# Optimization experiments

Hardware: AMD Instinct MI355X
Metric: run time of the kernel (lower is better)

## Reference

```python
import jax, jax.numpy as jnp
import numpy as np

N_NODES = 50000


def gcn_conv(x, src, dst, W, b):
    """PyG GCNConv: symmetric-normalized aggregation with self-loops.
    out[i] = sum_{j->i} deg^{-1/2}[j] deg^{-1/2}[i] (x_j @ W) + b
    src/dst already include self-loop edges.
    """
    n = x.shape[0]
    ew = jnp.ones(src.shape[0], dtype=x.dtype)
    deg = jax.ops.segment_sum(ew, dst, num_segments=n)  # [N]
    dinv = jnp.where(deg > 0, jax.lax.rsqrt(deg), 0.0).astype(x.dtype)
    norm = dinv[src] * dinv[dst]  # [E+N]
    xw = x @ W  # [N, z] dense transform first (as PyG does)
    msg = xw[src] * norm[:, None]  # gather + scale, [E+N, z]
    out = jax.ops.segment_sum(msg, dst, num_segments=n)  # scatter-add
    return out + b


def prelu(x, a):
    return jnp.where(x > 0, x, a * x)


def setup_inputs() -> dict:
    key = jax.random.key(0)
    k1, k2, k3, k4 = jax.random.split(key, 4)
    in_dim = z_dim = 96
    n_edges = 800000
    x = jax.random.normal(k1, (N_NODES, in_dim), dtype=jnp.float32)
    edge_index = jax.random.randint(k2, (2, n_edges), 0, N_NODES, dtype=jnp.int32)
    # Glorot-style init for GCN weights
    s1 = 1.0 / np.sqrt(in_dim)
    W1 = jax.random.uniform(k3, (in_dim, z_dim), jnp.float32, -s1, s1)
    W2 = jax.random.uniform(k4, (z_dim, z_dim), jnp.float32, -s1, s1)
    b1 = jnp.zeros((z_dim,), jnp.float32)
    b2 = jnp.zeros((z_dim,), jnp.float32)
    prelu_a = jnp.full((z_dim,), 0.25, jnp.float32)  # shared PReLU, per-channel
    return {"x": x, "edge_index": edge_index, "W1": W1, "b1": b1,
            "W2": W2, "b2": b2, "prelu_a": prelu_a}


def reference(x, edge_index, W1, b1, W2, b2, prelu_a):
    n = x.shape[0]
    loop = jnp.arange(n, dtype=edge_index.dtype)
    src = jnp.concatenate([edge_index[0], loop])
    dst = jnp.concatenate([edge_index[1], loop])
    h = prelu(gcn_conv(x, src, dst, W1, b1), prelu_a)
    h = prelu(gcn_conv(h, src, dst, W2, b2), prelu_a)
    return h
```

## Files before the change

### kernel.cpp

```cpp
#include <hip/hip_runtime.h>
#include <hip/hip_fp16.h>

#define D 96
#define D4 24
#define MAXBINS 256

static inline size_t alignup(size_t x) { return (x + 255) & ~size_t(255); }

__device__ inline float4 f4fma(float s, float4 a, float4 acc) {
    acc.x = fmaf(s, a.x, acc.x);
    acc.y = fmaf(s, a.y, acc.y);
    acc.z = fmaf(s, a.z, acc.z);
    acc.w = fmaf(s, a.w, acc.w);
    return acc;
}

__device__ inline void u4fma(uint4 rv, float w, float4& a0, float4& a1) {
    __half2 h0 = *reinterpret_cast<__half2*>(&rv.x);
    __half2 h1 = *reinterpret_cast<__half2*>(&rv.y);
    __half2 h2 = *reinterpret_cast<__half2*>(&rv.z);
    __half2 h3 = *reinterpret_cast<__half2*>(&rv.w);
    float2 f0 = __half22float2(h0);
    float2 f1 = __half22float2(h1);
    float2 f2 = __half22float2(h2);
    float2 f3 = __half22float2(h3);
    a0.x = fmaf(w, f0.x, a0.x);
    a0.y = fmaf(w, f0.y, a0.y);
    a0.z = fmaf(w, f1.x, a0.z);
    a0.w = fmaf(w, f1.y, a0.w);
    a1.x = fmaf(w, f2.x, a1.x);
    a1.y = fmaf(w, f2.y, a1.y);
    a1.z = fmaf(w, f3.x, a1.z);
    a1.w = fmaf(w, f3.y, a1.w);
}


__global__ __launch_bounds__(1024) void hist_kernel(const int* __restrict__ dst, int E,
                                                    int* __restrict__ bhist, int nbins) {
    __shared__ int h[MAXBINS];
    const int tid = threadIdx.x;
    if (tid < nbins) h[tid] = 0;
    __syncthreads();
    int e = blockIdx.x * 1024 + tid;
    if (e < E) atomicAdd(&h[dst[e] >> 8], 1);
    __syncthreads();
    if (tid < nbins) bhist[blockIdx.x * nbins + tid] = h[tid];
}

__global__ __launch_bounds__(1024) void scan1_kernel(const int* __restrict__ bhist,
                                                     int* __restrict__ boffs,
                                                     int* __restrict__ bsum,
                                                     int m, int nblk, int nbins) {
    __shared__ int wsum[16];
    const int i = blockIdx.x * 1024 + threadIdx.x;
    const int lane = threadIdx.x & 63;
    const int wid  = threadIdx.x >> 6;
    int v = 0;
    if (i < m) {
        int b = i % nblk, bin = i / nblk;
        v = bhist[b * nbins + bin];
    }
    int sc = v;
    #pragma unroll
    for (int off = 1; off < 64; off <<= 1) {
        int t = __shfl_up(sc, off);
        if (lane >= off) sc += t;
    }
    if (lane == 63) wsum[wid] = sc;
    __syncthreads();
    int wprefix = 0;
    #pragma unroll
    for (int k = 0; k < 16; ++k)
        if (k < wid) wprefix += wsum[k];
    if (i < m) boffs[i] = wprefix + (sc - v);
    if (threadIdx.x == 1023) bsum[blockIdx.x] = wprefix + sc;
}

__global__ __launch_bounds__(1024) void scan2_kernel(const int* __restrict__ bsum,
                                                     int* __restrict__ boff, int nb) {
    __shared__ int wsum[16];
    const int lane = threadIdx.x & 63;
    const int wid  = threadIdx.x >> 6;
    int v = ((int)threadIdx.x < nb) ? bsum[threadIdx.x] : 0;
    int sc = v;
    #pragma unroll
    for (int off = 1; off < 64; off <<= 1) {
        int t = __shfl_up(sc, off);
        if (lane >= off) sc += t;
    }
    if (lane == 63) wsum[wid] = sc;
    __syncthreads();
    int wprefix = 0;
    #pragma unroll
    for (int k = 0; k < 16; ++k)
        if (k < wid) wprefix += wsum[k];
    if ((int)threadIdx.x < nb) boff[threadIdx.x] = wprefix + (sc - v);
}

__global__ __launch_bounds__(1024) void dist_kernel(const int* __restrict__ src,
                                                    const int* __restrict__ dst, int E,
                                                    const int* __restrict__ boffs,
                                                    const int* __restrict__ bboff,
                                                    int nblk, int nbins,
                                                    int2* __restrict__ ebuf) {
    __shared__ int h[MAXBINS];
    __shared__ int base[MAXBINS];
    const int tid = threadIdx.x;
    if (tid < nbins) h[tid] = 0;
    __syncthreads();
    int e = blockIdx.x * 1024 + tid;
    int s = 0, d = 0, bin = 0, rank = 0;
    bool valid = e < E;
    if (valid) {
        s = src[e]; d = dst[e];
        bin = d >> 8;
        rank = atomicAdd(&h[bin], 1);
    }
    __syncthreads();
    if (tid < nbins) {
        int idx = tid * nblk + blockIdx.x;
        base[tid] = boffs[idx] + bboff[idx >> 10];
    }
    __syncthreads();
    if (valid) ebuf[base[bin] + rank] = make_int2(s, d);
}

__global__ __launch_bounds__(256) void bucketA_kernel(const int2* __restrict__ ebuf,
                                                      const int* __restrict__ boffs,
                                                      const int* __restrict__ bboff,
                                                      int nblk, int nbins,
                                                      float* __restrict__ dinv,
                                                      int* __restrict__ rowptr,
                                                      int n, int E) {
    __shared__ int cnt[256];
    __shared__ int wsum[4];
    const int k = blockIdx.x;
    const int tid = threadIdx.x;
    int i0 = k * nblk, i1 = (k + 1) * nblk;
    const int bstart = boffs[i0] + bboff[i0 >> 10];
    const int bend = (k + 1 < nbins) ? (boffs[i1] + bboff[i1 >> 10]) : E;
    cnt[tid] = 0;
    __syncthreads();
    for (int e = bstart + tid; e < bend; e += 256)
        atomicAdd(&cnt[ebuf[e].y & 255], 1);
    __syncthreads();
    int v = cnt[tid];
    const int lane = tid & 63, wid = tid >> 6;
    int sc = v;
    #pragma unroll
    for (int off = 1; off < 64; off <<= 1) {
        int t = __shfl_up(sc, off);
        if (lane >= off) sc += t;
    }
    if (lane == 63) wsum[wid] = sc;
    __syncthreads();
    int wprefix = 0;
    #pragma unroll
    for (int w = 0; w < 4; ++w)
        if (w < wid) wprefix += wsum[w];
    int node = k * 256 + tid;
    if (node < n) {
        dinv[node] = rsqrtf((float)(v + 1));
        rowptr[node] = bstart + wprefix + (sc - v);
    }
    if (k == nbins - 1 && tid == 0) rowptr[n] = E;
}

__global__ __launch_bounds__(256) void bucketB_kernel(const int2* __restrict__ ebuf,
                                                      const int* __restrict__ boffs,
                                                      const int* __restrict__ bboff,
                                                      int nblk, int nbins,
                                                      const int* __restrict__ rowptr,
                                                      const float* __restrict__ dinv,
                                                      int2* __restrict__ csr, int n, int E) {
    __shared__ int cur[256];
    const int k = blockIdx.x;
    const int tid = threadIdx.x;
    int i0 = k * nblk, i1 = (k + 1) * nblk;
    const int bstart = boffs[i0] + bboff[i0 >> 10];
    const int bend = (k + 1 < nbins) ? (boffs[i1] + bboff[i1 >> 10]) : E;
    int node = k * 256 + tid;
    cur[tid] = (node < n) ? rowptr[node] : 0;
    __syncthreads();
    for (int e = bstart + tid; e < bend; e += 256) {
        int2 ed = ebuf[e];
        int pos = atomicAdd(&cur[ed.y & 255], 1);
        csr[pos] = make_int2(ed.x, __float_as_int(dinv[ed.x]));
    }
}


__global__ __launch_bounds__(192) void matmul_kernel(const float* __restrict__ X,
                                                     const float* __restrict__ W,
                                                     uint2* __restrict__ Y, int n) {
    __shared__ float XsT[96 * 64];
    const int t = threadIdx.x;
    const int y = threadIdx.y;
    const int tid = y * 24 + t;
    const int row0 = blockIdx.x * 64;
    const float4* X4 = (const float4*)X;

    for (int i = tid; i < 64 * 24; i += 192) {
        int r = i / 24, c4 = i % 24;
        float4 v = make_float4(0.f, 0.f, 0.f, 0.f);
        if (row0 + r < n) v = X4[(size_t)(row0 + r) * D4 + c4];
        int rs = r ^ ((c4 & 15) << 2);
        XsT[(c4 * 4 + 0) * 64 + rs] = v.x;
        XsT[(c4 * 4 + 1) * 64 + rs] = v.y;
        XsT[(c4 * 4 + 2) * 64 + rs] = v.z;
        XsT[(c4 * 4 + 3) * 64 + rs] = v.w;
    }
    __syncthreads();

    const float4* W4 = (const float4*)W;
    float4 acc[8];
    #pragma unroll
    for (int r = 0; r < 8; ++r) acc[r] = make_float4(0.f, 0.f, 0.f, 0.f);
    const int rbase = y * 8;

    #pragma unroll 8
    for (int k = 0; k < 96; ++k) {
        float4 w = W4[k * D4 + t];
        int base0 = (rbase ^ (((k >> 2) & 15) << 2));
        float4 xa = *(const float4*)&XsT[k * 64 + base0];
        float4 xb = *(const float4*)&XsT[k * 64 + (base0 ^ 4)];
        acc[0] = f4fma(xa.x, w, acc[0]);
        acc[1] = f4fma(xa.y, w, acc[1]);
        acc[2] = f4fma(xa.z, w, acc[2]);
        acc[3] = f4fma(xa.w, w, acc[3]);
        acc[4] = f4fma(xb.x, w, acc[4]);
        acc[5] = f4fma(xb.y, w, acc[5]);
        acc[6] = f4fma(xb.z, w, acc[6]);
        acc[7] = f4fma(xb.w, w, acc[7]);
    }

    #pragma unroll
    for (int r = 0; r < 8; ++r) {
        int row = row0 + rbase + r;
        if (row < n) {
            __half2 ha = __float22half2_rn(make_float2(acc[r].x, acc[r].y));
            __half2 hb = __float22half2_rn(make_float2(acc[r].z, acc[r].w));
            uint2 st;
            st.x = *reinterpret_cast<unsigned int*>(&ha);
            st.y = *reinterpret_cast<unsigned int*>(&hb);
            Y[(size_t)row * D4 + t] = st;
        }
    }
}

__global__ __launch_bounds__(384) void aggregate_kernel(const uint4* __restrict__ XH4,
                                                        const int2* __restrict__ csr,
                                                        const int* __restrict__ rowptr,
                                                        const float* __restrict__ dinv,
                                                        const float4* __restrict__ b4,
                                                        const float4* __restrict__ pa4,
                                                        float4* __restrict__ out4, int n) {
    const int i = blockIdx.x * 32 + threadIdx.y;
    const int t = threadIdx.x;
    if (i >= n) return;
    const int beg = rowptr[i], end = rowptr[i + 1];
    float4 a0 = make_float4(0.f, 0.f, 0.f, 0.f);
    float4 a1 = make_float4(0.f, 0.f, 0.f, 0.f);
    int p = beg;
    for (; p + 8 <= end; p += 8) {
        int2 e0 = csr[p + 0];
        int2 e1 = csr[p + 1];
        int2 e2 = csr[p + 2];
        int2 e3 = csr[p + 3];
        int2 e4 = csr[p + 4];
        int2 e5 = csr[p + 5];
        int2 e6 = csr[p + 6];
        int2 e7 = csr[p + 7];
        uint4 r0 = XH4[(size_t)e0.x * 12 + t];
        uint4 r1 = XH4[(size_t)e1.x * 12 + t];
        uint4 r2 = XH4[(size_t)e2.x * 12 + t];
        uint4 r3 = XH4[(size_t)e3.x * 12 + t];
        uint4 r4 = XH4[(size_t)e4.x * 12 + t];
        uint4 r5 = XH4[(size_t)e5.x * 12 + t];
        uint4 r6 = XH4[(size_t)e6.x * 12 + t];
        uint4 r7 = XH4[(size_t)e7.x * 12 + t];
        u4fma(r0, __int_as_float(e0.y), a0, a1);
        u4fma(r1, __int_as_float(e1.y), a0, a1);
        u4fma(r2, __int_as_float(e2.y), a0, a1);
        u4fma(r3, __int_as_float(e3.y), a0, a1);
        u4fma(r4, __int_as_float(e4.y), a0, a1);
        u4fma(r5, __int_as_float(e5.y), a0, a1);
        u4fma(r6, __int_as_float(e6.y), a0, a1);
        u4fma(r7, __int_as_float(e7.y), a0, a1);
    }
    if (p + 4 <= end) {
        int2 e0 = csr[p + 0];
        int2 e1 = csr[p + 1];
        int2 e2 = csr[p + 2];
        int2 e3 = csr[p + 3];
        uint4 r0 = XH4[(size_t)e0.x * 12 + t];
        uint4 r1 = XH4[(size_t)e1.x * 12 + t];
        uint4 r2 = XH4[(size_t)e2.x * 12 + t];
        uint4 r3 = XH4[(size_t)e3.x * 12 + t];
        u4fma(r0, __int_as_float(e0.y), a0, a1);
        u4fma(r1, __int_as_float(e1.y), a0, a1);
        u4fma(r2, __int_as_float(e2.y), a0, a1);
        u4fma(r3, __int_as_float(e3.y), a0, a1);
        p += 4;
    }
    for (; p < end; ++p) {
        int2 e = csr[p];
        u4fma(XH4[(size_t)e.x * 12 + t], __int_as_float(e.y), a0, a1);
    }
    const float di = dinv[i];
    float4 s0 = make_float4(0.f, 0.f, 0.f, 0.f);
    float4 s1 = make_float4(0.f, 0.f, 0.f, 0.f);
    u4fma(XH4[(size_t)i * 12 + t], 1.f, s0, s1);
    float4 b0 = b4[2 * t], b1 = b4[2 * t + 1];
    float4 q0 = pa4[2 * t], q1 = pa4[2 * t + 1];
    float4 v0, v1;
    v0.x = fmaf(di, a0.x, di * di * s0.x) + b0.x;
    v0.y = fmaf(di, a0.y, di * di * s0.y) + b0.y;
    v0.z = fmaf(di, a0.z, di * di * s0.z) + b0.z;
    v0.w = fmaf(di, a0.w, di * di * s0.w) + b0.w;
    v1.x = fmaf(di, a1.x, di * di * s1.x) + b1.x;
    v1.y = fmaf(di, a1.y, di * di * s1.y) + b1.y;
    v1.z = fmaf(di, a1.z, di * di * s1.z) + b1.z;
    v1.w = fmaf(di, a1.w, di * di * s1.w) + b1.w;
    v0.x = v0.x > 0.f ? v0.x : q0.x * v0.x;
    v0.y = v0.y > 0.f ? v0.y : q0.y * v0.y;
    v0.z = v0.z > 0.f ? v0.z : q0.z * v0.z;
    v0.w = v0.w > 0.f ? v0.w : q0.w * v0.w;
    v1.x = v1.x > 0.f ? v1.x : q1.x * v1.x;
    v1.y = v1.y > 0.f ? v1.y : q1.y * v1.y;
    v1.z = v1.z > 0.f ? v1.z : q1.z * v1.z;
    v1.w = v1.w > 0.f ? v1.w : q1.w * v1.w;
    out4[(size_t)i * D4 + 2 * t] = v0;
    out4[(size_t)i * D4 + 2 * t + 1] = v1;
}

extern "C" void kernel_launch(void* const* d_in, const int* in_sizes, int n_in,
                              void* d_out, int out_size, void* d_ws, size_t ws_size,
                              hipStream_t stream) {
    const float* x   = (const float*)d_in[0];
    const int*   ei  = (const int*)d_in[1];
    const float* W1  = (const float*)d_in[2];
    const float* b1  = (const float*)d_in[3];
    const float* W2  = (const float*)d_in[4];
    const float* b2  = (const float*)d_in[5];
    const float* pa  = (const float*)d_in[6];
    const int n = in_sizes[0] / D;
    const int E = in_sizes[1] / 2;
    const int* srcp = ei;
    const int* dstp = ei + E;

    const int nbins  = (n + 255) / 256;
    const int nblk_e = (E + 1023) / 1024;
    const int m      = nbins * nblk_e;
    const int nbscan = (m + 1023) / 1024;

    char* w = (char*)d_ws;
    int*   bhist  = (int*)w;   w += alignup((size_t)m * 4);
    int*   boffs  = (int*)w;   w += alignup((size_t)m * 4);
    int*   bsum   = (int*)w;   w += alignup(1024 * 4);
    int*   bboff  = (int*)w;   w += alignup(1024 * 4);
    float* dinv   = (float*)w; w += alignup((size_t)n * 4);
    int*   rowptr = (int*)w;   w += alignup((size_t)(n + 1) * 4);
    int2*  ebuf   = (int2*)w;  w += alignup((size_t)E * 8);
    int2*  csr    = (int2*)w;  w += alignup((size_t)E * 8);
    uint4* xw     = (uint4*)w; w += alignup((size_t)n * D * 2);
    float* out    = (float*)d_out;

    hist_kernel<<<nblk_e, 1024, 0, stream>>>(dstp, E, bhist, nbins);
    scan1_kernel<<<nbscan, 1024, 0, stream>>>(bhist, boffs, bsum, m, nblk_e, nbins);
    scan2_kernel<<<1, 1024, 0, stream>>>(bsum, bboff, nbscan);
    dist_kernel<<<nblk_e, 1024, 0, stream>>>(srcp, dstp, E, boffs, bboff, nblk_e, nbins, ebuf);
    bucketA_kernel<<<nbins, 256, 0, stream>>>(ebuf, boffs, bboff, nblk_e, nbins,
                                              dinv, rowptr, n, E);
    bucketB_kernel<<<nbins, 256, 0, stream>>>(ebuf, boffs, bboff, nblk_e, nbins,
                                              rowptr, dinv, csr, n, E);

    dim3 mblk(24, 8);
    const int mgrid = (n + 63) / 64;
    dim3 ablk(12, 32);
    const int agrid = (n + 31) / 32;

    matmul_kernel<<<mgrid, mblk, 0, stream>>>(x, W1, (uint2*)xw, n);
    aggregate_kernel<<<agrid, ablk, 0, stream>>>(xw, csr, rowptr, dinv,
                                                 (const float4*)b1, (const float4*)pa, (float4*)out, n);
    matmul_kernel<<<mgrid, mblk, 0, stream>>>(out, W2, (uint2*)xw, n);
    aggregate_kernel<<<agrid, ablk, 0, stream>>>(xw, csr, rowptr, dinv,
                                                 (const float4*)b2, (const float4*)pa, (float4*)out, n);
}
```

Measured before the change: 148.4 us.

## Fold source normalization into matmul, slim CSR, merge bucket passes, degree-sort rows

Each matmul now scales its output rows by dinv, so the aggregation becomes a plain sum with a single dinv multiply at the end. The per-edge weight is dropped from the CSR (int instead of int2), and the edge buffer is split into a 4-byte source plus a 1-byte local destination. The two bucket kernels are merged into one. A degree histogram and permutation are added so aggregate blocks process rows of similar degree together, meant to reduce wave divergence. This adds two small kernels and a perm indirection, and fp16 now stores pre-scaled values.

```diff
diff --git a/kernel.cpp b/kernel.cpp
--- a/kernel.cpp
+++ b/kernel.cpp
@@ -15,7 +15,7 @@
     return acc;
 }
 
-__device__ inline void u4fma(uint4 rv, float w, float4& a0, float4& a1) {
+__device__ inline void u4add(uint4 rv, float4& a0, float4& a1) {
     __half2 h0 = *reinterpret_cast<__half2*>(&rv.x);
     __half2 h1 = *reinterpret_cast<__half2*>(&rv.y);
     __half2 h2 = *reinterpret_cast<__half2*>(&rv.z);
@@ -24,14 +24,8 @@
     float2 f1 = __half22float2(h1);
     float2 f2 = __half22float2(h2);
     float2 f3 = __half22float2(h3);
-    a0.x = fmaf(w, f0.x, a0.x);
-    a0.y = fmaf(w, f0.y, a0.y);
-    a0.z = fmaf(w, f1.x, a0.z);
-    a0.w = fmaf(w, f1.y, a0.w);
-    a1.x = fmaf(w, f2.x, a1.x);
-    a1.y = fmaf(w, f2.y, a1.y);
-    a1.z = fmaf(w, f3.x, a1.z);
-    a1.w = fmaf(w, f3.y, a1.w);
+    a0.x += f0.x; a0.y += f0.y; a0.z += f1.x; a0.w += f1.y;
+    a1.x += f2.x; a1.y += f2.y; a1.z += f3.x; a1.w += f3.y;
 }
 
 
@@ -77,8 +71,10 @@
 }
 
 __global__ __launch_bounds__(1024) void scan2_kernel(const int* __restrict__ bsum,
-                                                     int* __restrict__ boff, int nb) {
+                                                     int* __restrict__ boff, int nb,
+                                                     int* __restrict__ dhist_z) {
     __shared__ int wsum[16];
+    dhist_z[threadIdx.x] = 0;
     const int lane = threadIdx.x & 63;
     const int wid  = threadIdx.x >> 6;
     int v = ((int)threadIdx.x < nb) ? bsum[threadIdx.x] : 0;
@@ -102,7 +98,8 @@
                                                     const int* __restrict__ boffs,
                                                     const int* __restrict__ bboff,
                                                     int nblk, int nbins,
-                                                    int2* __restrict__ ebuf) {
+                                                    int* __restrict__ esrc,
+                                                    unsigned char* __restrict__ ed8) {
     __shared__ int h[MAXBINS];
     __shared__ int base[MAXBINS];
     const int tid = threadIdx.x;
@@ -122,27 +119,38 @@
         base[tid] = boffs[idx] + bboff[idx >> 10];
     }
     __syncthreads();
-    if (valid) ebuf[base[bin] + rank] = make_int2(s, d);
-}
-
-__global__ __launch_bounds__(256) void bucketA_kernel(const int2* __restrict__ ebuf,
-                                                      const int* __restrict__ boffs,
-                                                      const int* __restrict__ bboff,
-                                                      int nblk, int nbins,
-                                                      float* __restrict__ dinv,
-                                                      int* __restrict__ rowptr,
-                                                      int n, int E) {
+    if (valid) {
+        int pos = base[bin] + rank;
+        esrc[pos] = s;
+        ed8[pos] = (unsigned char)(d & 255);
+    }
+}
+
+__global__ __launch_bounds__(256) void bucketAB_kernel(const int* __restrict__ esrc,
+                                                       const unsigned char* __restrict__ ed8,
+                                                       const int* __restrict__ boffs,
+                                                       const int* __restrict__ bboff,
+                                                       int nblk, int nbins,
+                                                       float* __restrict__ dinv,
+                                                       int* __restrict__ rowptr,
+                                                       int* __restrict__ csr,
+                                                       int* __restrict__ dhist,
+                                                       unsigned char* __restrict__ deg8,
+                                                       int n, int E) {
     __shared__ int cnt[256];
+    __shared__ int cur[256];
     __shared__ int wsum[4];
+    __shared__ int dh[64];
     const int k = blockIdx.x;
     const int tid = threadIdx.x;
     int i0 = k * nblk, i1 = (k + 1) * nblk;
     const int bstart = boffs[i0] + bboff[i0 >> 10];
     const int bend = (k + 1 < nbins) ? (boffs[i1] + bboff[i1 >> 10]) : E;
     cnt[tid] = 0;
+    if (tid < 64) dh[tid] = 0;
     __syncthreads();
     for (int e = bstart + tid; e < bend; e += 256)
-        atomicAdd(&cnt[ebuf[e].y & 255], 1);
+        atomicAdd(&cnt[ed8[e]], 1);
     __syncthreads();
     int v = cnt[tid];
     const int lane = tid & 63, wid = tid >> 6;
@@ -158,40 +166,62 @@
     #pragma unroll
     for (int w = 0; w < 4; ++w)
         if (w < wid) wprefix += wsum[w];
+    int mybase = bstart + wprefix + (sc - v);
     int node = k * 256 + tid;
+    int dbin = v < 63 ? v : 63;
     if (node < n) {
         dinv[node] = rsqrtf((float)(v + 1));
-        rowptr[node] = bstart + wprefix + (sc - v);
+        rowptr[node] = mybase;
+        deg8[node] = (unsigned char)dbin;
+        atomicAdd(&dh[dbin], 1);
     }
     if (k == nbins - 1 && tid == 0) rowptr[n] = E;
-}
-
-__global__ __launch_bounds__(256) void bucketB_kernel(const int2* __restrict__ ebuf,
-                                                      const int* __restrict__ boffs,
-                                                      const int* __restrict__ bboff,
-                                                      int nblk, int nbins,
-                                                      const int* __restrict__ rowptr,
-                                                      const float* __restrict__ dinv,
-                                                      int2* __restrict__ csr, int n, int E) {
-    __shared__ int cur[256];
-    const int k = blockIdx.x;
+    cur[tid] = mybase;
+    __syncthreads();
+    if (tid < 64 && dh[tid]) atomicAdd(&dhist[tid * 16], dh[tid]);
+    for (int e = bstart + tid; e < bend; e += 256) {
+        int pos = atomicAdd(&cur[ed8[e]], 1);
+        csr[pos] = esrc[e];
+    }
+}
+
+__global__ __launch_bounds__(64) void dscan_kernel(const int* __restrict__ dhist,
+                                                   int* __restrict__ dcur) {
+    int v = dhist[threadIdx.x * 16];
+    int sc = v;
+    #pragma unroll
+    for (int off = 1; off < 64; off <<= 1) {
+        int t = __shfl_up(sc, off);
+        if ((int)threadIdx.x >= off) sc += t;
+    }
+    dcur[threadIdx.x * 16] = sc - v;
+}
+
+__global__ __launch_bounds__(1024) void dplace_kernel(const unsigned char* __restrict__ deg8,
+                                                      int* __restrict__ dcur,
+                                                      int* __restrict__ perm, int n) {
+    __shared__ int h[64];
+    __shared__ int base[64];
     const int tid = threadIdx.x;
-    int i0 = k * nblk, i1 = (k + 1) * nblk;
-    const int bstart = boffs[i0] + bboff[i0 >> 10];
-    const int bend = (k + 1 < nbins) ? (boffs[i1] + bboff[i1 >> 10]) : E;
-    int node = k * 256 + tid;
-    cur[tid] = (node < n) ? rowptr[node] : 0;
-    __syncthreads();
-    for (int e = bstart + tid; e < bend; e += 256) {
-        int2 ed = ebuf[e];
-        int pos = atomicAdd(&cur[ed.y & 255], 1);
-        csr[pos] = make_int2(ed.x, __float_as_int(dinv[ed.x]));
-    }
+    if (tid < 64) h[tid] = 0;
+    __syncthreads();
+    int i = blockIdx.x * 1024 + tid;
+    int bin = 0, rank = 0;
+    bool valid = i < n;
+    if (valid) {
+        bin = deg8[i];
+        rank = atomicAdd(&h[bin], 1);
+    }
+    __syncthreads();
+    if (tid < 64 && h[tid]) base[tid] = atomicAdd(&dcur[tid * 16], h[tid]);
+    __syncthreads();
+    if (valid) perm[base[bin] + rank] = i;
 }
 
 
 __global__ __launch_bounds__(192) void matmul_kernel(const float* __restrict__ X,
                                                      const float* __restrict__ W,
+                                                     const float* __restrict__ dinv,
                                                      uint2* __restrict__ Y, int n) {
     __shared__ float XsT[96 * 64];
     const int t = threadIdx.x;
@@ -238,8 +268,9 @@
     for (int r = 0; r < 8; ++r) {
         int row = row0 + rbase + r;
         if (row < n) {
-            __half2 ha = __float22half2_rn(make_float2(acc[r].x, acc[r].y));
-            __half2 hb = __float22half2_rn(make_float2(acc[r].z, acc[r].w));
+            float sc = dinv[row];
+            __half2 ha = __float22half2_rn(make_float2(sc * acc[r].x, sc * acc[r].y));
+            __half2 hb = __float22half2_rn(make_float2(sc * acc[r].z, sc * acc[r].w));
             uint2 st;
             st.x = *reinterpret_cast<unsigned int*>(&ha);
             st.y = *reinterpret_cast<unsigned int*>(&hb);
@@ -249,79 +280,77 @@
 }
 
 __global__ __launch_bounds__(384) void aggregate_kernel(const uint4* __restrict__ XH4,
-                                                        const int2* __restrict__ csr,
+                                                        const int* __restrict__ csr,
                                                         const int* __restrict__ rowptr,
                                                         const float* __restrict__ dinv,
+                                                        const int* __restrict__ perm,
                                                         const float4* __restrict__ b4,
                                                         const float4* __restrict__ pa4,
                                                         float4* __restrict__ out4, int n) {
-    const int i = blockIdx.x * 32 + threadIdx.y;
+    const int j = blockIdx.x * 32 + threadIdx.y;
     const int t = threadIdx.x;
-    if (i >= n) return;
+    if (j >= n) return;
+    const int i = perm[j];
     const int beg = rowptr[i], end = rowptr[i + 1];
     float4 a0 = make_float4(0.f, 0.f, 0.f, 0.f);
     float4 a1 = make_float4(0.f, 0.f, 0.f, 0.f);
     int p = beg;
     for (; p + 8 <= end; p += 8) {
-        int2 e0 = csr[p + 0];
-        int2 e1 = csr[p + 1];
-        int2 e2 = csr[p + 2];
-        int2 e3 = csr[p + 3];
-        int2 e4 = csr[p + 4];
-        int2 e5 = csr[p + 5];
-        int2 e6 = csr[p + 6];
-        int2 e7 = csr[p + 7];
-        uint4 r0 = XH4[(size_t)e0.x * 12 + t];
-        uint4 r1 = XH4[(size_t)e1.x * 12 + t];
-        uint4 r2 = XH4[(size_t)e2.x * 12 + t];
-        uint4 r3 = XH4[(size_t)e3.x * 12 + t];
-        uint4 r4 = XH4[(size_t)e4.x * 12 + t];
-        uint4 r5 = XH4[(size_t)e5.x * 12 + t];
-        uint4 r6 = XH4[(size_t)e6.x * 12 + t];
-        uint4 r7 = XH4[(size_t)e7.x * 12 + t];
-        u4fma(r0, __int_as_float(e0.y), a0, a1);
-        u4fma(r1, __int_as_float(e1.y), a0, a1);
-        u4fma(r2, __int_as_float(e2.y), a0, a1);
-        u4fma(r3, __int_as_float(e3.y), a0, a1);
-        u4fma(r4, __int_as_float(e4.y), a0, a1);
-        u4fma(r5, __int_as_float(e5.y), a0, a1);
-        u4fma(r6, __int_as_float(e6.y), a0, a1);
-        u4fma(r7, __int_as_float(e7.y), a0, a1);
+        int s0 = csr[p + 0];
+        int s1 = csr[p + 1];
+        int s2 = csr[p + 2];
+        int s3 = csr[p + 3];
+        int s4 = csr[p + 4];
+        int s5 = csr[p + 5];
+        int s6 = csr[p + 6];
+        int s7 = csr[p + 7];
+        uint4 r0 = XH4[(size_t)s0 * 12 + t];
+        uint4 r1 = XH4[(size_t)s1 * 12 + t];
+        uint4 r2 = XH4[(size_t)s2 * 12 + t];
+        uint4 r3 = XH4[(size_t)s3 * 12 + t];
+        uint4 r4 = XH4[(size_t)s4 * 12 + t];
+        uint4 r5 = XH4[(size_t)s5 * 12 + t];
+        uint4 r6 = XH4[(size_t)s6 * 12 + t];
+        uint4 r7 = XH4[(size_t)s7 * 12 + t];
+        u4add(r0, a0, a1);
+        u4add(r1, a0, a1);
+        u4add(r2, a0, a1);
+        u4add(r3, a0, a1);
+        u4add(r4, a0, a1);
+        u4add(r5, a0, a1);
+        u4add(r6, a0, a1);
+        u4add(r7, a0, a1);
     }
     if (p + 4 <= end) {
-        int2 e0 = csr[p + 0];
-        int2 e1 = csr[p + 1];
-        int2 e2 = csr[p + 2];
-        int2 e3 = csr[p + 3];
-        uint4 r0 = XH4[(size_t)e0.x * 12 + t];
-        uint4 r1 = XH4[(size_t)e1.x * 12 + t];
-        uint4 r2 = XH4[(size_t)e2.x * 12 + t];
-        uint4 r3 = XH4[(size_t)e3.x * 12 + t];
-        u4fma(r0, __int_as_float(e0.y), a0, a1);
-        u4fma(r1, __int_as_float(e1.y), a0, a1);
-        u4fma(r2, __int_as_float(e2.y), a0, a1);
-        u4fma(r3, __int_as_float(e3.y), a0, a1);
+        int s0 = csr[p + 0];
+        int s1 = csr[p + 1];
+        int s2 = csr[p + 2];
+        int s3 = csr[p + 3];
+        uint4 r0 = XH4[(size_t)s0 * 12 + t];
+        uint4 r1 = XH4[(size_t)s1 * 12 + t];
+        uint4 r2 = XH4[(size_t)s2 * 12 + t];
+        uint4 r3 = XH4[(size_t)s3 * 12 + t];
+        u4add(r0, a0, a1);
+        u4add(r1, a0, a1);
+        u4add(r2, a0, a1);
+        u4add(r3, a0, a1);
         p += 4;
     }
-    for (; p < end; ++p) {
-        int2 e = csr[p];
-        u4fma(XH4[(size_t)e.x * 12 + t], __int_as_float(e.y), a0, a1);
-    }
+    for (; p < end; ++p)
+        u4add(XH4[(size_t)csr[p] * 12 + t], a0, a1);
+    u4add(XH4[(size_t)i * 12 + t], a0, a1);
     const float di = dinv[i];
-    float4 s0 = make_float4(0.f, 0.f, 0.f, 0.f);
-    float4 s1 = make_float4(0.f, 0.f, 0.f, 0.f);
-    u4fma(XH4[(size_t)i * 12 + t], 1.f, s0, s1);
     float4 b0 = b4[2 * t], b1 = b4[2 * t + 1];
     float4 q0 = pa4[2 * t], q1 = pa4[2 * t + 1];
     float4 v0, v1;
-    v0.x = fmaf(di, a0.x, di * di * s0.x) + b0.x;
-    v0.y = fmaf(di, a0.y, di * di * s0.y) + b0.y;
-    v0.z = fmaf(di, a0.z, di * di * s0.z) + b0.z;
-    v0.w = fmaf(di, a0.w, di * di * s0.w) + b0.w;
-    v1.x = fmaf(di, a1.x, di * di * s1.x) + b1.x;
-    v1.y = fmaf(di, a1.y, di * di * s1.y) + b1.y;
-    v1.z = fmaf(di, a1.z, di * di * s1.z) + b1.z;
-    v1.w = fmaf(di, a1.w, di * di * s1.w) + b1.w;
+    v0.x = fmaf(di, a0.x, b0.x);
+    v0.y = fmaf(di, a0.y, b0.y);
+    v0.z = fmaf(di, a0.z, b0.z);
+    v0.w = fmaf(di, a0.w, b0.w);
+    v1.x = fmaf(di, a1.x, b1.x);
+    v1.y = fmaf(di, a1.y, b1.y);
+    v1.z = fmaf(di, a1.z, b1.z);
+    v1.w = fmaf(di, a1.w, b1.w);
     v0.x = v0.x > 0.f ? v0.x : q0.x * v0.x;
     v0.y = v0.y > 0.f ? v0.y : q0.y * v0.y;
     v0.z = v0.z > 0.f ? v0.z : q0.z * v0.z;
@@ -353,37 +382,44 @@
     const int nblk_e = (E + 1023) / 1024;
     const int m      = nbins * nblk_e;
     const int nbscan = (m + 1023) / 1024;
+    const int nbn    = (n + 1023) / 1024;
 
     char* w = (char*)d_ws;
     int*   bhist  = (int*)w;   w += alignup((size_t)m * 4);
     int*   boffs  = (int*)w;   w += alignup((size_t)m * 4);
     int*   bsum   = (int*)w;   w += alignup(1024 * 4);
     int*   bboff  = (int*)w;   w += alignup(1024 * 4);
+    int*   dhist  = (int*)w;   w += alignup(1024 * 4);
+    int*   dcur   = (int*)w;   w += alignup(1024 * 4);
     float* dinv   = (float*)w; w += alignup((size_t)n * 4);
     int*   rowptr = (int*)w;   w += alignup((size_t)(n + 1) * 4);
-    int2*  ebuf   = (int2*)w;  w += alignup((size_t)E * 8);
-    int2*  csr    = (int2*)w;  w += alignup((size_t)E * 8);
+    int*   perm   = (int*)w;   w += alignup((size_t)n * 4);
+    unsigned char* deg8 = (unsigned char*)w; w += alignup((size_t)n);
+    int*   esrc   = (int*)w;   w += alignup((size_t)E * 4);
+    unsigned char* ed8 = (unsigned char*)w;  w += alignup((size_t)E);
+    int*   csr    = (int*)w;   w += alignup((size_t)E * 4);
     uint4* xw     = (uint4*)w; w += alignup((size_t)n * D * 2);
     float* out    = (float*)d_out;
 
     hist_kernel<<<nblk_e, 1024, 0, stream>>>(dstp, E, bhist, nbins);
     scan1_kernel<<<nbscan, 1024, 0, stream>>>(bhist, boffs, bsum, m, nblk_e, nbins);
-    scan2_kernel<<<1, 1024, 0, stream>>>(bsum, bboff, nbscan);
-    dist_kernel<<<nblk_e, 1024, 0, stream>>>(srcp, dstp, E, boffs, bboff, nblk_e, nbins, ebuf);
-    bucketA_kernel<<<nbins, 256, 0, stream>>>(ebuf, boffs, bboff, nblk_e, nbins,
-                                              dinv, rowptr, n, E);
-    bucketB_kernel<<<nbins, 256, 0, stream>>>(ebuf, boffs, bboff, nblk_e, nbins,
-                                              rowptr, dinv, csr, n, E);
+    scan2_kernel<<<1, 1024, 0, stream>>>(bsum, bboff, nbscan, dhist);
+    dist_kernel<<<nblk_e, 1024, 0, stream>>>(srcp, dstp, E, boffs, bboff, nblk_e, nbins,
+                                             esrc, ed8);
+    bucketAB_kernel<<<nbins, 256, 0, stream>>>(esrc, ed8, boffs, bboff, nblk_e, nbins,
+                                               dinv, rowptr, csr, dhist, deg8, n, E);
+    dscan_kernel<<<1, 64, 0, stream>>>(dhist, dcur);
+    dplace_kernel<<<nbn, 1024, 0, stream>>>(deg8, dcur, perm, n);
 
     dim3 mblk(24, 8);
     const int mgrid = (n + 63) / 64;
     dim3 ablk(12, 32);
     const int agrid = (n + 31) / 32;
 
-    matmul_kernel<<<mgrid, mblk, 0, stream>>>(x, W1, (uint2*)xw, n);
-    aggregate_kernel<<<agrid, ablk, 0, stream>>>(xw, csr, rowptr, dinv,
+    matmul_kernel<<<mgrid, mblk, 0, stream>>>(x, W1, dinv, (uint2*)xw, n);
+    aggregate_kernel<<<agrid, ablk, 0, stream>>>(xw, csr, rowptr, dinv, perm,
                                                  (const float4*)b1, (const float4*)pa, (float4*)out, n);
-    matmul_kernel<<<mgrid, mblk, 0, stream>>>(out, W2, (uint2*)xw, n);
-    aggregate_kernel<<<agrid, ablk, 0, stream>>>(xw, csr, rowptr, dinv,
+    matmul_kernel<<<mgrid, mblk, 0, stream>>>(out, W2, dinv, (uint2*)xw, n);
+    aggregate_kernel<<<agrid, ablk, 0, stream>>>(xw, csr, rowptr, dinv, perm,
                                                  (const float4*)b2, (const float4*)pa, (float4*)out, n);
 }
```

New measurement: 158.8 us. +7.1%, slower.
